# Optimization experiments

Measured on AMD Instinct MI355X. Metric: run time of the kernel, lower is better.

## Reference

```python
import jax, jax.numpy as jnp
from jax import lax
import numpy as np

EPS = 1e-5  # BatchNorm2d default eps

def _cbs(x, w, g, b, m, v, pad):
    # Conv2d(bias=False) + BatchNorm2d (eval mode, running stats) + SiLU
    y = lax.conv_general_dilated(x, w, (1, 1), [(pad, pad), (pad, pad)],
                                 dimension_numbers=('NCHW', 'OIHW', 'NCHW'))
    y = (y - m[None, :, None, None]) * (g / jnp.sqrt(v + EPS))[None, :, None, None] + b[None, :, None, None]
    return y * jax.nn.sigmoid(y)

def setup_inputs():
    key = jax.random.key(0)
    B, C1, C2, H, W = 2, 128, 128, 20, 20
    ks = iter(jax.random.split(key, 16))
    def wconv(o, i, s):
        return jax.random.normal(next(ks), (o, i, s, s), jnp.float32) / np.float32(np.sqrt(i * s * s))
    def bn(cdim):
        k1, k2 = jax.random.split(next(ks))
        g = jax.random.uniform(k1, (cdim,), jnp.float32, 0.5, 1.5)
        b = jax.random.normal(k2, (cdim,), jnp.float32) * 0.1
        return g, b, jnp.zeros((cdim,), jnp.float32), jnp.ones((cdim,), jnp.float32)
    inp = {'x': jax.random.normal(next(ks), (B, C1, H, W), jnp.float32)}
    inp['w1'] = wconv(C2, C1, 1); inp['g1'], inp['b1'], inp['m1'], inp['v1'] = bn(C2)
    inp['w2'] = wconv(C2, C1, 1); inp['g2'], inp['b2'], inp['m2'], inp['v2'] = bn(C2)
    inp['wr1'] = wconv(C2, 2 * C2, 1); inp['gr1'], inp['br1'], inp['mr1'], inp['vr1'] = bn(C2)
    inp['wr2'] = wconv(C2, C2, 3); inp['gr2'], inp['br2'], inp['mr2'], inp['vr2'] = bn(C2)
    inp['wr3'] = wconv(1, C2, 1); inp['gr3'], inp['br3'], inp['mr3'], inp['vr3'] = bn(1)
    return inp

def reference(x, w1, g1, b1, m1, v1, w2, g2, b2, m2, v2,
              wr1, gr1, br1, mr1, vr1, wr2, gr2, br2, mr2, vr2,
              wr3, gr3, br3, mr3, vr3):
    B, C, H, W = x.shape
    HW = H * W
    # feat: [B, HW, C2]
    feat = _cbs(x, w1, g1, b1, m1, v1, 0).reshape(B, -1, HW).transpose(0, 2, 1)
    C2 = feat.shape[-1]
    # pairwise concat: rel[b,i,j] = [feat[b,i], feat[b,j]]  -> [B, HW, HW, 2*C2]
    fi = jnp.broadcast_to(feat[:, :, None, :], (B, HW, HW, C2))
    fj = jnp.broadcast_to(feat[:, None, :, :], (B, HW, HW, C2))
    rel = jnp.concatenate([fi, fj], axis=-1)
    # faithful permute(0,3,1,2) + contiguous view to [B*HW, 2*C2, H, W]
    rel = rel.transpose(0, 3, 1, 2).reshape(B * HW, 2 * C2, H, W)
    r = _cbs(rel, wr1, gr1, br1, mr1, vr1, 0)
    r = _cbs(r, wr2, gr2, br2, mr2, vr2, 1)
    r = _cbs(r, wr3, gr3, br3, mr3, vr3, 0)  # [B*HW, 1, H, W]
    scores = r.reshape(B, HW, HW)
    # bmm aggregation then back to [B, C2, H, W]
    att = jnp.einsum('bij,bjc->bic', scores, feat).transpose(0, 2, 1).reshape(B, C2, H, W)
    return _cbs(att, w2, g2, b2, m2, v2, 0) + x
```

## Files before the change

kernel.cpp:

```cpp
#include <hip/hip_runtime.h>

#define EPS 1e-5f

typedef __bf16 bf16x8 __attribute__((ext_vector_type(8)));
typedef float  f32x4  __attribute__((ext_vector_type(4)));

__device__ __forceinline__ unsigned short f2bf(float f) {
  unsigned int u = __float_as_uint(f);
  unsigned int r = (u + 0x7fffu + ((u >> 16) & 1u)) >> 16;
  return (unsigned short)r;
}
__device__ __forceinline__ float silu(float y) {
  return y * __builtin_amdgcn_rcpf(1.f + __expf(-y));
}

__global__ void prep_kernel(const float* __restrict__ x, const float* __restrict__ w1,
                            const float* __restrict__ g1, const float* __restrict__ b1,
                            const float* __restrict__ m1, const float* __restrict__ v1,
                            const float* __restrict__ wr2, const float* __restrict__ wr1,
                            float* __restrict__ feat, float* __restrict__ featT,
                            unsigned short* __restrict__ Apack, float* __restrict__ Pfx,
                            float* __restrict__ Wt, float* __restrict__ wr1T) {
  int blk = blockIdx.x;
  int tid = threadIdx.x;
  if (blk < 400) {
    int hp = tid >> 7, c = tid & 127;
    int pp = blk * 2 + hp;
    int b = pp / 400, p = pp % 400;
    __shared__ float xv[2][128];
    xv[hp][c] = x[(b * 128 + c) * 400 + p];
    __syncthreads();
    const float4* w4 = (const float4*)(w1 + c * 128);
    const float4* v4 = (const float4*)xv[hp];
    float s0 = 0.f, s1 = 0.f, s2 = 0.f, s3 = 0.f;
#pragma unroll
    for (int i = 0; i < 32; ++i) {
      float4 wv = w4[i], xx = v4[i];
      s0 += wv.x * xx.x; s1 += wv.y * xx.y; s2 += wv.z * xx.z; s3 += wv.w * xx.w;
    }
    float s = (s0 + s1) + (s2 + s3);
    float sc = g1[c] * rsqrtf(v1[c] + EPS);
    float y = s * sc + (b1[c] - m1[c] * sc);
    float f = silu(y);
    feat[(b * 400 + p) * 128 + c] = f;
    featT[(b * 128 + c) * 400 + p] = f;
  } else if (blk < 472) {
    int f = (blk - 400) * 4 + (tid >> 6);
    int lane = tid & 63;
    int tap = f >> 5, ks = (f >> 3) & 3, m8 = f & 7;
    int o  = m8 * 16 + (lane & 15);
    int cb = ks * 32 + (lane >> 4) * 8;
    unsigned short* dst = Apack + ((size_t)f * 64 + lane) * 8;
#pragma unroll
    for (int j = 0; j < 8; ++j)
      dst[j] = f2bf(wr2[(o * 128 + (cb + j)) * 9 + tap]);
  } else if (blk < 504) {
    int o = (blk - 472) * 4 + (tid >> 6);
    int lane = tid & 63;
    float4 wv = ((const float4*)(wr1 + o * 256))[lane];
    float p0 = wv.x, p1 = p0 + wv.y, p2 = p1 + wv.z, p3 = p2 + wv.w;
    float v = p3;
#pragma unroll
    for (int d = 1; d < 64; d <<= 1) {
      float t = __shfl_up(v, d);
      if (lane >= d) v += t;
    }
    float off = v - p3;
    float* Po = Pfx + o * 257;
    if (lane == 0) Po[0] = 0.f;
    Po[lane * 4 + 1] = off + p0;
    Po[lane * 4 + 2] = off + p1;
    Po[lane * 4 + 3] = off + p2;
    Po[lane * 4 + 4] = off + p3;
  } else if (blk < 648) {
    int base = (blk - 504) * 1024;
#pragma unroll
    for (int k = 0; k < 4; ++k) {
      int idx = base + k * 256 + tid;
      int tap = idx >> 14;
      int r = idx & 16383;
      int i = r >> 7, o = r & 127;
      Wt[idx] = wr2[(o * 128 + i) * 9 + tap];
    }
  } else {
    int base = (blk - 648) * 1024;
#pragma unroll
    for (int k = 0; k < 4; ++k) {
      int idx = base + k * 256 + tid;
      int i = idx >> 7, o = idx & 127;
      wr1T[idx] = wr1[o * 256 + i];
    }
  }
}

__global__ __launch_bounds__(512, 4) void rel_kernel(
    const float* __restrict__ feat, const float* __restrict__ featT,
    const float* __restrict__ wr1T, const float* __restrict__ Pfx,
    const float* __restrict__ gr1, const float* __restrict__ br1,
    const float* __restrict__ mr1, const float* __restrict__ vr1,
    const unsigned short* __restrict__ Apack, const float* __restrict__ Wt,
    const float* __restrict__ gr2, const float* __restrict__ br2,
    const float* __restrict__ mr2, const float* __restrict__ vr2,
    const float* __restrict__ wr3,
    const float* __restrict__ gr3, const float* __restrict__ br3,
    const float* __restrict__ mr3, const float* __restrict__ vr3,
    const float* __restrict__ x, const float* __restrict__ w2,
    const float* __restrict__ g2, const float* __restrict__ b2,
    const float* __restrict__ m2, const float* __restrict__ v2,
    float* __restrict__ out) {

  __shared__ __align__(16) unsigned short r1f[16 * 221 * 8];
  __shared__ float f0s[220], f1s[220], scoreS[208];
  __shared__ float wB0s[128], wB1s[128];
  __shared__ float sc1[128], sh1[128], sc2[128], sh2[128], w3c[128];
  __shared__ __align__(16) float attT[128];
  __shared__ __align__(16) float fA[256];
  __shared__ float r1c[128], AvS[128];
  __shared__ float vS[9 * 128];
  __shared__ float spS[9];
  __shared__ float spP[400];

  int tid = threadIdx.x, lane = tid & 63, wid = tid >> 6;
  int blk = blockIdx.x;

  if (tid < 128) {
    float s1 = gr1[tid] * rsqrtf(vr1[tid] + EPS); sc1[tid] = s1; sh1[tid] = br1[tid] - mr1[tid] * s1;
    float s2 = gr2[tid] * rsqrtf(vr2[tid] + EPS); sc2[tid] = s2; sh2[tid] = br2[tid] - mr2[tid] * s2;
    w3c[tid] = wr3[tid];
    attT[tid] = 0.f; AvS[tid] = 0.f;
  }
  float s3 = gr3[0] * rsqrtf(vr3[0] + EPS);
  float sh3 = br3[0] - mr3[0] * s3;

  if (blk < 400) {
    int b = blk / 200, q = 200 + blk % 200;
    int c0 = (q * 256) / 400, c1 = c0 + 1;
    if (tid < 128) {
      const float* Po = Pfx + tid * 257;
      int e0 = min(256, 400 * c0 + 400 - 256 * q);
      wB0s[tid] = Po[e0];
      float wv = 0.f;
      if (c1 < 256) {
        int s1i = min(256, max(0, 400 * c1 - 256 * q));
        wv = Po[256] - Po[s1i];
      }
      wB1s[tid] = wv;
    }

    int wm = wid & 1, wn = wid >> 1;
    int ntcnt = (wn == 0) ? 4 : 3;
    int n16 = lane & 15, quad = lane >> 4;
    const char* wbase = (const char*)Apack + (size_t)((wm * 4) * 64 + lane) * 16;

#pragma unroll
    for (int half = 0; half < 2; ++half) {
      if (tid < 220) {
        int p = tid + 180 * half;
        f0s[tid] = featT[(b * 128 + (c0 - 128)) * 400 + p];
        f1s[tid] = (c1 < 256) ? featT[(b * 128 + (c1 - 128)) * 400 + p] : 0.f;
      }
      if (tid < 208) scoreS[tid] = 0.f;
      __syncthreads();

      for (int i = tid; i < 3520; i += 512) {
        int plane = i / 220, p = i - plane * 220;
        int cb = (plane >> 2) * 32 + (plane & 3) * 8;
        float fa0 = f0s[p], fa1 = f1s[p];
        unsigned int pk[4];
#pragma unroll
        for (int jp = 0; jp < 4; ++jp) {
          int c = cb + jp * 2;
          float y0 = wB0s[c] * fa0 + wB1s[c] * fa1;     y0 = y0 * sc1[c] + sh1[c];
          float y1 = wB0s[c + 1] * fa0 + wB1s[c + 1] * fa1; y1 = y1 * sc1[c + 1] + sh1[c + 1];
          pk[jp] = (unsigned int)f2bf(silu(y0)) | ((unsigned int)f2bf(silu(y1)) << 16);
        }
        *(uint4*)&r1f[(plane * 221 + p) * 8] = make_uint4(pk[0], pk[1], pk[2], pk[3]);
      }
      if (tid < 16) *(uint4*)&r1f[(tid * 221 + 220) * 8] = make_uint4(0, 0, 0, 0);

      int hA[4], wA[4], poA[4]; bool pov[4];
#pragma unroll
      for (int t = 0; t < 4; ++t) {
        int po = (wn + 4 * t) * 16 + n16;
        poA[t] = po; pov[t] = po < 200;
        int pg = half * 200 + po;
        hA[t] = pg / 20; wA[t] = pg - 20 * hA[t];
      }
      f32x4 acc[4][4];
#pragma unroll
      for (int mt = 0; mt < 4; ++mt)
#pragma unroll
        for (int t = 0; t < 4; ++t) acc[mt][t] = f32x4{0.f, 0.f, 0.f, 0.f};

      __syncthreads();

      for (int tap = 0; tap < 9; ++tap) {
        int dy = tap / 3 - 1, dx = tap % 3 - 1;
        int pp[4];
#pragma unroll
        for (int t = 0; t < 4; ++t) {
          int hh = hA[t] + dy, ww = wA[t] + dx;
          bool valid = pov[t] & (hh >= 0) & (hh < 20) & (ww >= 0) & (ww < 20);
          pp[t] = valid ? (hh - 9 * half) * 20 + ww : 220;
        }
#pragma unroll
        for (int ks = 0; ks < 4; ++ks) {
          const char* wp = wbase + (size_t)(tap * 4 + ks) * 8192;
          bf16x8 af0 = *(const bf16x8*)(wp);
          bf16x8 af1 = *(const bf16x8*)(wp + 1024);
          bf16x8 af2 = *(const bf16x8*)(wp + 2048);
          bf16x8 af3 = *(const bf16x8*)(wp + 3072);
          int pbase = (ks * 4 + quad) * 221;
#pragma unroll
          for (int t = 0; t < 4; ++t) {
            if (t < ntcnt) {
              bf16x8 bfr = *(const bf16x8*)&r1f[(pbase + pp[t]) * 8];
              acc[0][t] = __builtin_amdgcn_mfma_f32_16x16x32_bf16(af0, bfr, acc[0][t], 0, 0, 0);
              acc[1][t] = __builtin_amdgcn_mfma_f32_16x16x32_bf16(af1, bfr, acc[1][t], 0, 0, 0);
              acc[2][t] = __builtin_amdgcn_mfma_f32_16x16x32_bf16(af2, bfr, acc[2][t], 0, 0, 0);
              acc[3][t] = __builtin_amdgcn_mfma_f32_16x16x32_bf16(af3, bfr, acc[3][t], 0, 0, 0);
            }
          }
        }
      }

#pragma unroll
      for (int t = 0; t < 4; ++t) {
        if (t < ntcnt) {
          float ps = 0.f;
#pragma unroll
          for (int mt = 0; mt < 4; ++mt) {
#pragma unroll
            for (int r = 0; r < 4; ++r) {
              int o = wm * 64 + mt * 16 + quad * 4 + r;
              float y = acc[mt][t][r] * sc2[o] + sh2[o];
              ps += silu(y) * w3c[o];
            }
          }
          ps += __shfl_xor(ps, 16);
          ps += __shfl_xor(ps, 32);
          if (quad == 0 && pov[t]) atomicAdd(&scoreS[poA[t]], ps);
        }
      }
      __syncthreads();

      if (tid < 200) scoreS[tid] = silu(scoreS[tid] * s3 + sh3);
      __syncthreads();

      {
        int c = tid & 127, part = tid >> 7;
        float s = 0.f;
        int j0 = part * 50;
        const float* fb = feat + ((size_t)(b * 400 + half * 200 + j0)) * 128 + c;
#pragma unroll 10
        for (int j = 0; j < 50; ++j)
          s += scoreS[j0 + j] * fb[(size_t)j * 128];
        atomicAdd(&attT[c], s);
      }
      __syncthreads();
    }

    {
      int c = tid >> 2, sub = tid & 3;
      const float4* w4 = (const float4*)(w2 + c * 128 + sub * 32);
      const float4* v4 = (const float4*)(attT + sub * 32);
      float s0 = 0.f, s1 = 0.f, s2v = 0.f, s3v = 0.f;
#pragma unroll
      for (int i = 0; i < 8; ++i) {
        float4 wv = w4[i], xx = v4[i];
        s0 += wv.x * xx.x; s1 += wv.y * xx.y; s2v += wv.z * xx.z; s3v += wv.w * xx.w;
      }
      float s = (s0 + s1) + (s2v + s3v);
      s += __shfl_xor(s, 1);
      s += __shfl_xor(s, 2);
      if (sub == 0) {
        float scc = g2[c] * rsqrtf(v2[c] + EPS);
        float y = s * scc + (b2[c] - m2[c] * scc);
        int xi = (b * 128 + c) * 400 + q;
        out[xi] = silu(y) + x[xi];
      }
    }
  } else {
    int cidx = blk - 400;
    int b = cidx / 200, q = cidx % 200;
    if (tid < 256) {
      int u = q * 256 + tid; int c = u / 400, i2 = u - c * 400;
      fA[tid] = featT[(b * 128 + c) * 400 + i2];
    }
    for (int k = tid; k < 1152; k += 512) vS[k] = 0.f;
    __syncthreads();
    {
      int o = tid & 127, part = tid >> 7;
      const float* wt = wr1T + part * 64 * 128 + o;
      const float* fv = fA + part * 64;
      float a = 0.f;
#pragma unroll 8
      for (int k = 0; k < 64; ++k) a += wt[k * 128] * fv[k];
      atomicAdd(&AvS[o], a);
    }
    __syncthreads();
    if (tid < 128) r1c[tid] = silu(AvS[tid] * sc1[tid] + sh1[tid]);
    __syncthreads();
    {
      int o = tid & 127, part = tid >> 7;
      const float* rc = r1c + part * 32;
      for (int tap = 0; tap < 9; ++tap) {
        const float* wt = Wt + tap * 16384 + part * 32 * 128 + o;
        float s = 0.f;
#pragma unroll 8
        for (int i2 = 0; i2 < 32; ++i2) s += wt[i2 * 128] * rc[i2];
        atomicAdd(&vS[tap * 128 + o], s);
      }
    }
    __syncthreads();
    for (int pat = wid; pat < 9; pat += 8) {
      int ry = pat / 3, rx = pat % 3;
      float ps = 0.f;
      for (int oo = lane; oo < 128; oo += 64) {
        float y = 0.f;
#pragma unroll
        for (int dy = -1; dy <= 1; ++dy) {
          if ((ry == 0 && dy < 0) || (ry == 2 && dy > 0)) continue;
#pragma unroll
          for (int dx = -1; dx <= 1; ++dx) {
            if ((rx == 0 && dx < 0) || (rx == 2 && dx > 0)) continue;
            y += vS[((dy + 1) * 3 + (dx + 1)) * 128 + oo];
          }
        }
        y = y * sc2[oo] + sh2[oo];
        ps += silu(y) * w3c[oo];
      }
#pragma unroll
      for (int sft = 32; sft >= 1; sft >>= 1) ps += __shfl_xor(ps, sft);
      if (lane == 0) spS[pat] = silu(ps * s3 + sh3);
    }
    __syncthreads();

    for (int p = tid; p < 400; p += 512) {
      int r = p / 20, cm = p - 20 * r;
      int ry = (r == 0) ? 0 : (r == 19) ? 2 : 1;
      int rx = (cm == 0) ? 0 : (cm == 19) ? 2 : 1;
      spP[p] = spS[ry * 3 + rx];
    }
    __syncthreads();
    {
      int c = tid & 127, part = tid >> 7;
      const float* fb = feat + ((size_t)(b * 400) + part * 100) * 128 + c;
      const float* sp = spP + part * 100;
      float s = 0.f;
#pragma unroll 10
      for (int j = 0; j < 100; ++j) s += sp[j] * fb[(size_t)j * 128];
      atomicAdd(&attT[c], s);
    }
    __syncthreads();
    {
      int c = tid >> 2, sub = tid & 3;
      const float4* w4 = (const float4*)(w2 + c * 128 + sub * 32);
      const float4* v4 = (const float4*)(attT + sub * 32);
      float s0 = 0.f, s1 = 0.f, s2v = 0.f, s3v = 0.f;
#pragma unroll
      for (int i = 0; i < 8; ++i) {
        float4 wv = w4[i], xx = v4[i];
        s0 += wv.x * xx.x; s1 += wv.y * xx.y; s2v += wv.z * xx.z; s3v += wv.w * xx.w;
      }
      float s = (s0 + s1) + (s2v + s3v);
      s += __shfl_xor(s, 1);
      s += __shfl_xor(s, 2);
      if (sub == 0) {
        float scc = g2[c] * rsqrtf(v2[c] + EPS);
        float y = s * scc + (b2[c] - m2[c] * scc);
        int xi = (b * 128 + c) * 400 + q;
        out[xi] = silu(y) + x[xi];
      }
    }
  }
}

extern "C" void kernel_launch(void* const* d_in, const int* in_sizes, int n_in,
                              void* d_out, int out_size, void* d_ws, size_t ws_size,
                              hipStream_t stream) {
  const float* x   = (const float*)d_in[0];
  const float* w1  = (const float*)d_in[1];
  const float* g1  = (const float*)d_in[2];
  const float* b1  = (const float*)d_in[3];
  const float* m1  = (const float*)d_in[4];
  const float* v1  = (const float*)d_in[5];
  const float* w2  = (const float*)d_in[6];
  const float* g2  = (const float*)d_in[7];
  const float* b2  = (const float*)d_in[8];
  const float* m2  = (const float*)d_in[9];
  const float* v2  = (const float*)d_in[10];
  const float* wr1 = (const float*)d_in[11];
  const float* gr1 = (const float*)d_in[12];
  const float* br1 = (const float*)d_in[13];
  const float* mr1 = (const float*)d_in[14];
  const float* vr1 = (const float*)d_in[15];
  const float* wr2 = (const float*)d_in[16];
  const float* gr2 = (const float*)d_in[17];
  const float* br2 = (const float*)d_in[18];
  const float* mr2 = (const float*)d_in[19];
  const float* vr2 = (const float*)d_in[20];
  const float* wr3 = (const float*)d_in[21];
  const float* gr3 = (const float*)d_in[22];
  const float* br3 = (const float*)d_in[23];
  const float* mr3 = (const float*)d_in[24];
  const float* vr3 = (const float*)d_in[25];
  float* out = (float*)d_out;

  char* ws = (char*)d_ws;
  float*          feat  = (float*)ws;
  unsigned short* Apack = (unsigned short*)(ws + 819200);
  float*          Pfx   = (float*)(ws + 1114112);
  float*          Wt    = (float*)(ws + 1245696);
  float*          featT = (float*)(ws + 1901056);
  float*          wr1T  = (float*)(ws + 2310656);

  prep_kernel<<<680, 256, 0, stream>>>(x, w1, g1, b1, m1, v1, wr2, wr1,
                                       feat, featT, Apack, Pfx, Wt, wr1T);
  rel_kernel<<<800, 512, 0, stream>>>(feat, featT, wr1T, Pfx, gr1, br1, mr1, vr1,
                                      Apack, Wt,
                                      gr2, br2, mr2, vr2, wr3, gr3, br3, mr3, vr3,
                                      x, w2, g2, b2, m2, v2, out);
}
```

Baseline: 199.3 us.

## Stage weights through shared memory in prep kernel and batch feat pixels per block

The 1x1 conv for feat now runs 8 pixels per block with w1 staged in padded LDS, which cuts the block count from 400 to 100 and reuses weights across pixels. The wr2 and wr1 repack and transpose branches now do coalesced float4 loads into LDS before the strided gather, replacing scattered global reads. The grid shrinks from 680 to 380 blocks. Every block now declares about 74 KB of static shared memory, which may lower occupancy for the smaller branches.

Result: faster. 193.0 us (-3.2%).

```diff
diff --git a/kernel.cpp b/kernel.cpp
--- a/kernel.cpp
+++ b/kernel.cpp
@@ -21,41 +21,71 @@
                             float* __restrict__ feat, float* __restrict__ featT,
                             unsigned short* __restrict__ Apack, float* __restrict__ Pfx,
                             float* __restrict__ Wt, float* __restrict__ wr1T) {
+  __shared__ __align__(16) float sbuf[18496];
   int blk = blockIdx.x;
   int tid = threadIdx.x;
-  if (blk < 400) {
-    int hp = tid >> 7, c = tid & 127;
-    int pp = blk * 2 + hp;
-    int b = pp / 400, p = pp % 400;
-    __shared__ float xv[2][128];
-    xv[hp][c] = x[(b * 128 + c) * 400 + p];
-    __syncthreads();
-    const float4* w4 = (const float4*)(w1 + c * 128);
-    const float4* v4 = (const float4*)xv[hp];
-    float s0 = 0.f, s1 = 0.f, s2 = 0.f, s3 = 0.f;
-#pragma unroll
-    for (int i = 0; i < 32; ++i) {
-      float4 wv = w4[i], xx = v4[i];
-      s0 += wv.x * xx.x; s1 += wv.y * xx.y; s2 += wv.z * xx.z; s3 += wv.w * xx.w;
-    }
-    float s = (s0 + s1) + (s2 + s3);
+  if (blk < 100) {
+    float* w1s = sbuf;
+    float* xvb = sbuf + 16512;
+    int p0 = blk * 8;
+    int b = p0 / 400, pb = p0 % 400;
+    const float4* w14 = (const float4*)w1;
+    for (int u = tid; u < 4096; u += 256) {
+      float4 v = w14[u];
+      int c = u >> 5, i4 = (u & 31) * 4;
+      float* d = w1s + c * 129 + i4;
+      d[0] = v.x; d[1] = v.y; d[2] = v.z; d[3] = v.w;
+    }
+    for (int u = tid; u < 1024; u += 256) {
+      int pl = u >> 7, c = u & 127;
+      xvb[pl * 128 + c] = x[(b * 128 + c) * 400 + pb + pl];
+    }
+    __syncthreads();
+    int c = tid & 127, pg = tid >> 7;
+    float a0[4], a1[4], a2[4], a3[4];
+#pragma unroll
+    for (int q = 0; q < 4; ++q) { a0[q] = a1[q] = a2[q] = a3[q] = 0.f; }
+    const float* wr = w1s + c * 129;
+#pragma unroll 8
+    for (int k = 0; k < 32; ++k) {
+      float w0 = wr[4 * k], w1v = wr[4 * k + 1], w2v = wr[4 * k + 2], w3v = wr[4 * k + 3];
+#pragma unroll
+      for (int q = 0; q < 4; ++q) {
+        float4 xx = *(const float4*)&xvb[(pg * 4 + q) * 128 + 4 * k];
+        a0[q] += w0 * xx.x; a1[q] += w1v * xx.y; a2[q] += w2v * xx.z; a3[q] += w3v * xx.w;
+      }
+    }
     float sc = g1[c] * rsqrtf(v1[c] + EPS);
-    float y = s * sc + (b1[c] - m1[c] * sc);
-    float f = silu(y);
-    feat[(b * 400 + p) * 128 + c] = f;
-    featT[(b * 128 + c) * 400 + p] = f;
-  } else if (blk < 472) {
-    int f = (blk - 400) * 4 + (tid >> 6);
-    int lane = tid & 63;
-    int tap = f >> 5, ks = (f >> 3) & 3, m8 = f & 7;
-    int o  = m8 * 16 + (lane & 15);
-    int cb = ks * 32 + (lane >> 4) * 8;
+    float sh = b1[c] - m1[c] * sc;
+#pragma unroll
+    for (int q = 0; q < 4; ++q) {
+      float s = (a0[q] + a1[q]) + (a2[q] + a3[q]);
+      float f = silu(s * sc + sh);
+      int p = pb + pg * 4 + q;
+      feat[(b * 400 + p) * 128 + c] = f;
+      featT[(b * 128 + c) * 400 + p] = f;
+    }
+  } else if (blk < 172) {
+    int w_ = blk - 100;
+    int tap = w_ >> 3, ks = (w_ >> 1) & 3, o0 = (w_ & 1) * 64;
+    const float4* s4 = (const float4*)wr2;
+    for (int u = tid; u < 4608; u += 256) {
+      int o = u / 72, r = u - o * 72;
+      float4 v = s4[(size_t)(o0 + o) * 288 + 72 * ks + r];
+      float* d = sbuf + o * 289 + r * 4;
+      d[0] = v.x; d[1] = v.y; d[2] = v.z; d[3] = v.w;
+    }
+    __syncthreads();
+    int wv = tid >> 6, lane = tid & 63;
+    int f = w_ * 4 + wv;
+    int o_l = wv * 16 + (lane & 15);
+    int ib = (lane >> 4) * 8;
     unsigned short* dst = Apack + ((size_t)f * 64 + lane) * 8;
 #pragma unroll
     for (int j = 0; j < 8; ++j)
-      dst[j] = f2bf(wr2[(o * 128 + (cb + j)) * 9 + tap]);
-  } else if (blk < 504) {
-    int o = (blk - 472) * 4 + (tid >> 6);
+      dst[j] = f2bf(sbuf[o_l * 289 + (ib + j) * 9 + tap]);
+  } else if (blk < 204) {
+    int o = (blk - 172) * 4 + (tid >> 6);
     int lane = tid & 63;
     float4 wv = ((const float4*)(wr1 + o * 256))[lane];
     float p0 = wv.x, p1 = p0 + wv.y, p2 = p1 + wv.z, p3 = p2 + wv.w;
@@ -72,23 +102,43 @@
     Po[lane * 4 + 2] = off + p1;
     Po[lane * 4 + 3] = off + p2;
     Po[lane * 4 + 4] = off + p3;
-  } else if (blk < 648) {
-    int base = (blk - 504) * 1024;
+  } else if (blk < 348) {
+    int blk_ = blk - 204;
+    int base = blk_ * 1024;
+    int tap = blk_ >> 4;
+    int i0 = (blk_ & 15) * 8;
+    const float4* s4 = (const float4*)wr2;
+    int i0q = (9 * i0) >> 2;
+    for (int u = tid; u < 2304; u += 256) {
+      int o = u / 18, r = u - o * 18;
+      float4 v = s4[o * 288 + i0q + r];
+      float* d = sbuf + o * 73 + r * 4;
+      d[0] = v.x; d[1] = v.y; d[2] = v.z; d[3] = v.w;
+    }
+    __syncthreads();
 #pragma unroll
     for (int k = 0; k < 4; ++k) {
       int idx = base + k * 256 + tid;
-      int tap = idx >> 14;
-      int r = idx & 16383;
-      int i = r >> 7, o = r & 127;
-      Wt[idx] = wr2[(o * 128 + i) * 9 + tap];
+      int o = idx & 127, il = ((idx & 16383) >> 7) - i0;
+      Wt[idx] = sbuf[o * 73 + il * 9 + tap];
     }
   } else {
-    int base = (blk - 648) * 1024;
+    int blk_ = blk - 348;
+    int base = blk_ * 1024;
+    int i0 = base >> 7;
+    const float4* s4 = (const float4*)wr1;
+    {
+      int o = tid >> 1, r = tid & 1;
+      float4 v = s4[o * 64 + (i0 >> 2) + r];
+      float* d = sbuf + o * 9 + r * 4;
+      d[0] = v.x; d[1] = v.y; d[2] = v.z; d[3] = v.w;
+    }
+    __syncthreads();
 #pragma unroll
     for (int k = 0; k < 4; ++k) {
       int idx = base + k * 256 + tid;
-      int i = idx >> 7, o = idx & 127;
-      wr1T[idx] = wr1[o * 256 + i];
+      int o = idx & 127, il = (idx >> 7) - i0;
+      wr1T[idx] = sbuf[o * 9 + il];
     }
   }
 }
@@ -415,7 +465,7 @@
   float*          featT = (float*)(ws + 1901056);
   float*          wr1T  = (float*)(ws + 2310656);
 
-  prep_kernel<<<680, 256, 0, stream>>>(x, w1, g1, b1, m1, v1, wr2, wr1,
+  prep_kernel<<<380, 256, 0, stream>>>(x, w1, g1, b1, m1, v1, wr2, wr1,
                                        feat, featT, Apack, Pfx, Wt, wr1T);
   rel_kernel<<<800, 512, 0, stream>>>(feat, featT, wr1T, Pfx, gr1, br1, mr1, vr1,
                                       Apack, Wt,
```
